# Performance work log

Measured on AMD Instinct MI355X. Metric: run time of the kernel, lower is better.

Reference implementation:

```python
import jax, jax.numpy as jnp
import numpy as np

NEG_SLOPE = 0.2  # PyG GATConv default negative_slope


def _add_self_loops(edge_index, num_nodes):
    # PyG GATConv add_self_loops=True default
    loop = jnp.arange(num_nodes, dtype=edge_index.dtype)
    src = jnp.concatenate([edge_index[0], loop])
    dst = jnp.concatenate([edge_index[1], loop])
    return src, dst


def _gat_layer(x, src, dst, W, att_src, att_dst, bias, heads, out_ch):
    """One PyG-style GATConv layer (concat=True).
    x: [N, F_in]; W: [F_in, heads*out_ch]; att_*: [heads, out_ch]; bias: [heads*out_ch].
    """
    N = x.shape[0]
    h = (x @ W).reshape(N, heads, out_ch)               # [N, H, C]
    a_src = jnp.einsum('nhc,hc->nh', h, att_src)        # [N, H]
    a_dst = jnp.einsum('nhc,hc->nh', h, att_dst)        # [N, H]
    logits = jax.nn.leaky_relu(a_src[src] + a_dst[dst], NEG_SLOPE)  # [E, H]
    # segment softmax over destination neighborhoods
    m = jax.ops.segment_max(logits, dst, num_segments=N)            # [N, H]
    e = jnp.exp(logits - m[dst])                                     # [E, H]
    s = jax.ops.segment_sum(e, dst, num_segments=N)                  # [N, H]
    alpha = e / s[dst]                                               # [E, H]
    # scatter-aggregate weighted source features
    out = jax.ops.segment_sum(alpha[:, :, None] * h[src], dst, num_segments=N)  # [N, H, C]
    return out.reshape(N, heads * out_ch) + bias


def setup_inputs() -> dict:
    key = jax.random.key(0)
    ks = jax.random.split(key, 10)
    N, E = 50000, 800000
    F_in, HID, H, NC = 128, 64, 4, 10
    x = jax.random.normal(ks[0], (N, F_in), dtype=jnp.float32)
    edge_index = jax.random.randint(ks[1], (2, E), 0, N, dtype=jnp.int64)
    sc1 = 1.0 / np.sqrt(F_in)
    sc2 = 1.0 / np.sqrt(HID * H)
    return {
        'x': x,
        'edge_index': edge_index,
        'W1': jax.random.normal(ks[2], (F_in, H * HID), dtype=jnp.float32) * sc1,
        'att_src1': jax.random.normal(ks[3], (H, HID), dtype=jnp.float32) * sc1,
        'att_dst1': jax.random.normal(ks[4], (H, HID), dtype=jnp.float32) * sc1,
        'b1': jnp.zeros((H * HID,), dtype=jnp.float32),
        'W2': jax.random.normal(ks[5], (H * HID, NC), dtype=jnp.float32) * sc2,
        'att_src2': jax.random.normal(ks[6], (1, NC), dtype=jnp.float32) * sc2,
        'att_dst2': jax.random.normal(ks[7], (1, NC), dtype=jnp.float32) * sc2,
        'b2': jnp.zeros((NC,), dtype=jnp.float32),
    }


def reference(x, edge_index, W1, att_src1, att_dst1, b1, W2, att_src2, att_dst2, b2):
    N = x.shape[0]
    src, dst = _add_self_loops(edge_index, N)
    h = _gat_layer(x, src, dst, W1, att_src1, att_dst1, b1, heads=4, out_ch=64)
    h = jax.nn.elu(h)
    out = _gat_layer(h, src, dst, W2, att_src2, att_dst2, b2, heads=1, out_ch=10)
    return out
```

## Files before the change

### kernel.cpp

```cpp
#include <hip/hip_runtime.h>
#include <hip/hip_fp16.h>
#include <math.h>

#define NEG_SLOPE 0.2f
#define LOG2E 1.44269504088896f

#if __has_builtin(__builtin_amdgcn_exp2f)
#define EXP2(x) __builtin_amdgcn_exp2f(x)
#else
#define EXP2(x) exp2f(x)
#endif

typedef _Float16 half8 __attribute__((ext_vector_type(8)));
typedef float floatx4 __attribute__((ext_vector_type(4)));

__global__ __launch_bounds__(256) void prep1(const float* __restrict__ W1,
                                             half8* __restrict__ Bpack,
                                             int* __restrict__ deg, int N) {
  if (blockIdx.x < 16) {
    int tid = blockIdx.x * 256 + threadIdx.x;
    int l = tid & 63;
    int ksnt = tid >> 6;
    int ks = ksnt & 3;
    int nt = ksnt >> 2;
    int col = nt * 16 + (l & 15);
    int krow = ks * 32 + (l >> 4) * 8;
    half8 v;
#pragma unroll
    for (int j = 0; j < 8; j++) v[j] = (_Float16)W1[(krow + j) * 256 + col];
    Bpack[tid] = v;
  } else {
    int i = (blockIdx.x - 16) * 256 + threadIdx.x;
    if (i < N) deg[i] = 0;
  }
}

__global__ __launch_bounds__(256) void phase2(
    const float* __restrict__ x, const half8* __restrict__ Bpack,
    const float* __restrict__ att_s, const float* __restrict__ att_d,
    __half* __restrict__ h1, float* __restrict__ a1s, float* __restrict__ a1d,
    const int* __restrict__ dst, int* __restrict__ deg,
    int N, int E, int gemmBlocks, int histBlocks) {
  if ((int)blockIdx.x >= gemmBlocks) {
    int b = blockIdx.x - gemmBlocks;
    for (int e = b * 256 + threadIdx.x; e < E; e += histBlocks * 256)
      atomicAdd(deg + dst[e], 1);
    return;
  }
  const int wave = threadIdx.x >> 6, lane = threadIdx.x & 63;
  const int quad = lane >> 4, li = lane & 15;
  const int n0 = (blockIdx.x * 4 + wave) * 16;
  if (n0 >= N) return;
  floatx4 acc[16];
#pragma unroll
  for (int t = 0; t < 16; t++) acc[t] = (floatx4){0.f, 0.f, 0.f, 0.f};
  const float* xrow = x + (size_t)(n0 + li) * 128;
#pragma unroll
  for (int ks = 0; ks < 4; ks++) {
    float4 xa = *(const float4*)(xrow + ks * 32 + quad * 8);
    float4 xb = *(const float4*)(xrow + ks * 32 + quad * 8 + 4);
    half8 a;
    a[0] = (_Float16)xa.x; a[1] = (_Float16)xa.y;
    a[2] = (_Float16)xa.z; a[3] = (_Float16)xa.w;
    a[4] = (_Float16)xb.x; a[5] = (_Float16)xb.y;
    a[6] = (_Float16)xb.z; a[7] = (_Float16)xb.w;
#pragma unroll
    for (int nt = 0; nt < 16; nt++) {
      half8 b = Bpack[(nt * 4 + ks) * 64 + lane];
      acc[nt] = __builtin_amdgcn_mfma_f32_16x16x32_f16(a, b, acc[nt], 0, 0, 0);
    }
  }
#pragma unroll
  for (int nt = 0; nt < 16; nt++) {
#pragma unroll
    for (int r = 0; r < 4; r++) {
      h1[(size_t)(n0 + quad * 4 + r) * 256 + nt * 16 + li] = __float2half(acc[nt][r]);
    }
  }
  float as_f[16], ad_f[16];
#pragma unroll
  for (int nt = 0; nt < 16; nt++) {
    as_f[nt] = att_s[nt * 16 + li];
    ad_f[nt] = att_d[nt * 16 + li];
  }
#pragma unroll
  for (int r = 0; r < 4; r++) {
    int node = n0 + quad * 4 + r;
#pragma unroll
    for (int h = 0; h < 4; h++) {
      float vs = 0.f, vd = 0.f;
#pragma unroll
      for (int ntl = 0; ntl < 4; ntl++) {
        int nt = h * 4 + ntl;
        vs = fmaf(acc[nt][r], as_f[nt], vs);
        vd = fmaf(acc[nt][r], ad_f[nt], vd);
      }
#pragma unroll
      for (int off = 8; off > 0; off >>= 1) {
        vs += __shfl_down(vs, off, 16);
        vd += __shfl_down(vd, off, 16);
      }
      if (li == 0) {
        a1s[node * 4 + h] = vs * LOG2E;
        a1d[node * 4 + h] = vd * LOG2E;
      }
    }
  }
}

__global__ void scan_local(const int* __restrict__ deg, int* __restrict__ excl,
                           int* __restrict__ bsum, int N) {
  __shared__ int s[256];
  int i = blockIdx.x * 256 + threadIdx.x;
  int v = (i < N) ? deg[i] + 1 : 0;
  s[threadIdx.x] = v;
  __syncthreads();
  for (int off = 1; off < 256; off <<= 1) {
    int t = (threadIdx.x >= off) ? s[threadIdx.x - off] : 0;
    __syncthreads();
    s[threadIdx.x] += t;
    __syncthreads();
  }
  if (i < N) excl[i] = s[threadIdx.x] - v;
  if (threadIdx.x == 255) bsum[blockIdx.x] = s[255];
}

__global__ void scan_bsum(int* __restrict__ bsum, int nb) {
  __shared__ int s[256];
  int v = (threadIdx.x < nb) ? bsum[threadIdx.x] : 0;
  s[threadIdx.x] = v;
  __syncthreads();
  for (int off = 1; off < 256; off <<= 1) {
    int t = (threadIdx.x >= off) ? s[threadIdx.x - off] : 0;
    __syncthreads();
    s[threadIdx.x] += t;
    __syncthreads();
  }
  if (threadIdx.x < nb) bsum[threadIdx.x] = s[threadIdx.x] - v;
}

__global__ void scan_add(const int* __restrict__ excl, const int* __restrict__ bsum,
                         int* __restrict__ rowptr, int* __restrict__ cursor,
                         int* __restrict__ elist, int N, int ET) {
  int i = blockIdx.x * 256 + threadIdx.x;
  if (i < N) {
    int r = excl[i] + bsum[blockIdx.x];
    rowptr[i] = r;
    elist[r] = i;
    cursor[i] = r + 1;
  }
  if (i == 0) rowptr[N] = ET;
}

__global__ void scatter_edges(const int* __restrict__ src, const int* __restrict__ dst,
                              int* __restrict__ cursor, int* __restrict__ elist, int E) {
  int e = blockIdx.x * 256 + threadIdx.x;
  if (e >= E) return;
  int pos = atomicAdd(cursor + dst[e], 1);
  elist[pos] = src[e];
}

__global__ __launch_bounds__(256) void agg1_fused(
    const int* __restrict__ rowptr, const int* __restrict__ elist,
    const __half* __restrict__ h1, const float* __restrict__ a1s,
    const float* __restrict__ a1d, const float* __restrict__ b1,
    const float* __restrict__ W2, const float* __restrict__ as2,
    const float* __restrict__ ad2, __half* __restrict__ h2,
    float* __restrict__ a2s, float* __restrict__ a2d, int N) {
  __shared__ float w2s[64 * 41];
  const int t = threadIdx.x;
  for (int i = t; i < 2560; i += 256) {
    int ch = i / 10, jj = i - ch * 10;
    w2s[(ch >> 2) * 41 + (ch & 3) * 10 + jj] = W2[i];
  }
  __syncthreads();

  const int wave = t >> 6, lane = t & 63;
  const int n = blockIdx.x * 4 + wave;
  if (n >= N) return;
  const int row = rowptr[n];
  const int deg = rowptr[n + 1] - row;
  const int* el = elist + row;
  const int hidx = lane >> 4;
  const float adh = a1d[n * 4 + hidx];

  float den = 0.f;
  float acc0 = 0.f, acc1 = 0.f, acc2 = 0.f, acc3 = 0.f;
  int j = 0;
  for (; j + 8 <= deg; j += 8) {
    int ss[8];
#pragma unroll
    for (int u = 0; u < 8; u++) ss[u] = el[j + u];
    float lv[8];
    uint2 uv[8];
#pragma unroll
    for (int u = 0; u < 8; u++) {
      lv[u] = a1s[ss[u] * 4 + hidx];
      uv[u] = *(const uint2*)(h1 + (size_t)ss[u] * 256 + lane * 4);
    }
#pragma unroll
    for (int u = 0; u < 8; u++) {
      float l = lv[u] + adh;
      float e = EXP2(fmaxf(l, NEG_SLOPE * l));
      den += e;
      float2 a = __half22float2(*(const __half2*)&uv[u].x);
      float2 b = __half22float2(*(const __half2*)&uv[u].y);
      acc0 = fmaf(e, a.x, acc0); acc1 = fmaf(e, a.y, acc1);
      acc2 = fmaf(e, b.x, acc2); acc3 = fmaf(e, b.y, acc3);
    }
  }
  for (; j + 4 <= deg; j += 4) {
    int ss[4];
#pragma unroll
    for (int u = 0; u < 4; u++) ss[u] = el[j + u];
    float lv[4];
    uint2 uv[4];
#pragma unroll
    for (int u = 0; u < 4; u++) {
      lv[u] = a1s[ss[u] * 4 + hidx];
      uv[u] = *(const uint2*)(h1 + (size_t)ss[u] * 256 + lane * 4);
    }
#pragma unroll
    for (int u = 0; u < 4; u++) {
      float l = lv[u] + adh;
      float e = EXP2(fmaxf(l, NEG_SLOPE * l));
      den += e;
      float2 a = __half22float2(*(const __half2*)&uv[u].x);
      float2 b = __half22float2(*(const __half2*)&uv[u].y);
      acc0 = fmaf(e, a.x, acc0); acc1 = fmaf(e, a.y, acc1);
      acc2 = fmaf(e, b.x, acc2); acc3 = fmaf(e, b.y, acc3);
    }
  }
  for (; j < deg; j++) {
    int s0 = el[j];
    float l0 = a1s[s0 * 4 + hidx] + adh;
    uint2 u0 = *(const uint2*)(h1 + (size_t)s0 * 256 + lane * 4);
    float e0 = EXP2(fmaxf(l0, NEG_SLOPE * l0));
    den += e0;
    float2 a = __half22float2(*(const __half2*)&u0.x);
    float2 b = __half22float2(*(const __half2*)&u0.y);
    acc0 = fmaf(e0, a.x, acc0); acc1 = fmaf(e0, a.y, acc1);
    acc2 = fmaf(e0, b.x, acc2); acc3 = fmaf(e0, b.y, acc3);
  }

  float inv = 1.0f / den;
  float4 bb = *(const float4*)(b1 + lane * 4);
  float c0 = fmaf(acc0, inv, bb.x);
  float c1 = fmaf(acc1, inv, bb.y);
  float c2 = fmaf(acc2, inv, bb.z);
  float c3 = fmaf(acc3, inv, bb.w);
  c0 = c0 > 0.f ? c0 : expm1f(c0);
  c1 = c1 > 0.f ? c1 : expm1f(c1);
  c2 = c2 > 0.f ? c2 : expm1f(c2);
  c3 = c3 > 0.f ? c3 : expm1f(c3);
  const float* w0 = w2s + lane * 41;
  float p[10];
#pragma unroll
  for (int jj = 0; jj < 10; jj++)
    p[jj] = fmaf(c0, w0[jj], fmaf(c1, w0[10 + jj], fmaf(c2, w0[20 + jj], c3 * w0[30 + jj])));
#pragma unroll
  for (int jj = 0; jj < 10; jj++) {
#pragma unroll
    for (int off = 32; off > 0; off >>= 1) p[jj] += __shfl_down(p[jj], off, 64);
  }
  if (lane == 0) {
    float ds = 0.f, dd = 0.f;
#pragma unroll
    for (int jj = 0; jj < 10; jj++) {
      h2[(size_t)n * 16 + jj] = __float2half(p[jj]);
      ds = fmaf(p[jj], as2[jj], ds);
      dd = fmaf(p[jj], ad2[jj], dd);
    }
    a2s[n] = ds * LOG2E;
    a2d[n] = dd * LOG2E;
  }
}

__global__ __launch_bounds__(256) void agg2_csr(
    const int* __restrict__ rowptr, const int* __restrict__ elist,
    const __half* __restrict__ h2, const float* __restrict__ a2s,
    const float* __restrict__ a2d, const float* __restrict__ b2,
    float* __restrict__ out, int N) {
  int wave = threadIdx.x >> 6, lane = threadIdx.x & 63;
  int n = blockIdx.x * 4 + wave;
  if (n >= N) return;
  int row = rowptr[n];
  int deg = rowptr[n + 1] - row;
  const int* el = elist + row;
  float ad = a2d[n];
  int g = lane / 10;
  int c = lane - g * 10;
  float den = 0.f, acc = 0.f;
  if (g < 6) {
    int jj = g;
    for (; jj + 6 < deg; jj += 12) {
      int sA = el[jj], sB = el[jj + 6];
      float lA = a2s[sA] + ad;
      float lB = a2s[sB] + ad;
      __half hA = h2[(size_t)sA * 16 + c];
      __half hB = h2[(size_t)sB * 16 + c];
      float eA = EXP2(fmaxf(lA, NEG_SLOPE * lA));
      float eB = EXP2(fmaxf(lB, NEG_SLOPE * lB));
      den += eA + eB;
      acc = fmaf(eA, __half2float(hA), fmaf(eB, __half2float(hB), acc));
    }
    for (; jj < deg; jj += 6) {
      int s = el[jj];
      float l = a2s[s] + ad;
      float ev = EXP2(fmaxf(l, NEG_SLOPE * l));
      den += ev;
      acc = fmaf(ev, __half2float(h2[(size_t)s * 16 + c]), acc);
    }
  }
  acc += __shfl_down(acc, 30, 64);
  den += __shfl_down(den, 30, 64);
  acc += __shfl_down(acc, 10, 64) + __shfl_down(acc, 20, 64);
  den += __shfl_down(den, 10, 64) + __shfl_down(den, 20, 64);
  if (lane < 10) out[(size_t)n * 10 + lane] = acc / den + b2[lane];
}

extern "C" void kernel_launch(void* const* d_in, const int* in_sizes, int n_in,
                              void* d_out, int out_size, void* d_ws, size_t ws_size,
                              hipStream_t stream) {
  const float* x = (const float*)d_in[0];
  const int* ei = (const int*)d_in[1];
  const float* W1 = (const float*)d_in[2];
  const float* as1 = (const float*)d_in[3];
  const float* ad1 = (const float*)d_in[4];
  const float* b1 = (const float*)d_in[5];
  const float* W2 = (const float*)d_in[6];
  const float* as2 = (const float*)d_in[7];
  const float* ad2 = (const float*)d_in[8];
  const float* b2 = (const float*)d_in[9];
  float* out = (float*)d_out;

  const int N = in_sizes[0] / 128;
  const int E = in_sizes[1] / 2;
  const int ET = E + N;
  const int* srcp = ei;
  const int* dstp = ei + E;

  char* ws = (char*)d_ws;
  size_t off = 0;
  auto alloc = [&](size_t nbytes) {
    char* p = ws + off;
    off += (nbytes + 255) & ~(size_t)255;
    return p;
  };
  __half* h1 = (__half*)alloc((size_t)N * 256 * 2);
  half8* Bpack = (half8*)alloc((size_t)4096 * 16);
  float* a1s = (float*)alloc((size_t)N * 4 * 4);
  float* a1d = (float*)alloc((size_t)N * 4 * 4);
  __half* h2 = (__half*)alloc((size_t)N * 16 * 2);
  float* a2sv = (float*)alloc((size_t)N * 4);
  float* a2dv = (float*)alloc((size_t)N * 4);
  int* deg = (int*)alloc((size_t)N * 4);
  int* excl = (int*)alloc((size_t)N * 4);
  int* bsum = (int*)alloc(256 * 4);
  int* rowptr = (int*)alloc((size_t)(N + 1) * 4);
  int* cursor = (int*)alloc((size_t)N * 4);
  int* elist = (int*)alloc((size_t)ET * 4);

  const int nb = (N + 255) / 256;
  const int gemmBlocks = (N / 16 + 3) / 4;
  const int histBlocks = 512;

  prep1<<<16 + nb, 256, 0, stream>>>(W1, Bpack, deg, N);
  phase2<<<gemmBlocks + histBlocks, 256, 0, stream>>>(
      x, Bpack, as1, ad1, h1, a1s, a1d, dstp, deg, N, E, gemmBlocks, histBlocks);
  scan_local<<<nb, 256, 0, stream>>>(deg, excl, bsum, N);
  scan_bsum<<<1, 256, 0, stream>>>(bsum, nb);
  scan_add<<<nb, 256, 0, stream>>>(excl, bsum, rowptr, cursor, elist, N, ET);
  scatter_edges<<<(E + 255) / 256, 256, 0, stream>>>(srcp, dstp, cursor, elist, E);
  agg1_fused<<<(N + 3) / 4, 256, 0, stream>>>(rowptr, elist, h1, a1s, a1d, b1, W2,
                                              as2, ad2, h2, a2sv, a2dv, N);
  agg2_csr<<<(N + 3) / 4, 256, 0, stream>>>(rowptr, elist, h2, a2sv, a2dv, b2, out, N);
}
```

Before: 295.9 us.

## Record atomic ranks in histogram, pad CSR rows, merge scan kernels

The degree histogram now stores each edge's atomicAdd return value as its rank. The scatter then writes edges directly to rowptr+1+rank, with no second atomic pass through a cursor array. Row lengths are padded to multiples of four so aggregation can read neighbor indices with aligned int4 loads. The block-sum scan is folded into the add kernel, which removes one launch. The cost is an extra E-sized rank array plus a larger elist, and the degree is read from the deg array rather than from rowptr differences.

```diff
diff --git a/kernel.cpp b/kernel.cpp
--- a/kernel.cpp
+++ b/kernel.cpp
@@ -39,12 +39,12 @@
     const float* __restrict__ x, const half8* __restrict__ Bpack,
     const float* __restrict__ att_s, const float* __restrict__ att_d,
     __half* __restrict__ h1, float* __restrict__ a1s, float* __restrict__ a1d,
-    const int* __restrict__ dst, int* __restrict__ deg,
+    const int* __restrict__ dst, int* __restrict__ deg, int* __restrict__ rank,
     int N, int E, int gemmBlocks, int histBlocks) {
   if ((int)blockIdx.x >= gemmBlocks) {
     int b = blockIdx.x - gemmBlocks;
     for (int e = b * 256 + threadIdx.x; e < E; e += histBlocks * 256)
-      atomicAdd(deg + dst[e], 1);
+      rank[e] = atomicAdd(deg + dst[e], 1);
     return;
   }
   const int wave = threadIdx.x >> 6, lane = threadIdx.x & 63;
@@ -112,7 +112,7 @@
                            int* __restrict__ bsum, int N) {
   __shared__ int s[256];
   int i = blockIdx.x * 256 + threadIdx.x;
-  int v = (i < N) ? deg[i] + 1 : 0;
+  int v = (i < N) ? ((deg[i] + 1 + 3) & ~3) : 0;
   s[threadIdx.x] = v;
   __syncthreads();
   for (int off = 1; off < 256; off <<= 1) {
@@ -125,7 +125,9 @@
   if (threadIdx.x == 255) bsum[blockIdx.x] = s[255];
 }
 
-__global__ void scan_bsum(int* __restrict__ bsum, int nb) {
+__global__ void scan_add2(const int* __restrict__ excl, const int* __restrict__ bsum,
+                          int* __restrict__ rowptr, int* __restrict__ elist,
+                          int N, int nb) {
   __shared__ int s[256];
   int v = (threadIdx.x < nb) ? bsum[threadIdx.x] : 0;
   s[threadIdx.x] = v;
@@ -136,37 +138,32 @@
     s[threadIdx.x] += t;
     __syncthreads();
   }
-  if (threadIdx.x < nb) bsum[threadIdx.x] = s[threadIdx.x] - v;
-}
-
-__global__ void scan_add(const int* __restrict__ excl, const int* __restrict__ bsum,
-                         int* __restrict__ rowptr, int* __restrict__ cursor,
-                         int* __restrict__ elist, int N, int ET) {
+  __syncthreads();
+  int base = (blockIdx.x > 0) ? s[blockIdx.x - 1] : 0;
   int i = blockIdx.x * 256 + threadIdx.x;
   if (i < N) {
-    int r = excl[i] + bsum[blockIdx.x];
+    int r = excl[i] + base;
     rowptr[i] = r;
     elist[r] = i;
-    cursor[i] = r + 1;
-  }
-  if (i == 0) rowptr[N] = ET;
-}
-
-__global__ void scatter_edges(const int* __restrict__ src, const int* __restrict__ dst,
-                              int* __restrict__ cursor, int* __restrict__ elist, int E) {
+  }
+}
+
+__global__ void scatter2(const int* __restrict__ src, const int* __restrict__ dst,
+                         const int* __restrict__ rank, const int* __restrict__ rowptr,
+                         int* __restrict__ elist, int E) {
   int e = blockIdx.x * 256 + threadIdx.x;
   if (e >= E) return;
-  int pos = atomicAdd(cursor + dst[e], 1);
-  elist[pos] = src[e];
+  elist[rowptr[dst[e]] + 1 + rank[e]] = src[e];
 }
 
 __global__ __launch_bounds__(256) void agg1_fused(
-    const int* __restrict__ rowptr, const int* __restrict__ elist,
-    const __half* __restrict__ h1, const float* __restrict__ a1s,
-    const float* __restrict__ a1d, const float* __restrict__ b1,
-    const float* __restrict__ W2, const float* __restrict__ as2,
-    const float* __restrict__ ad2, __half* __restrict__ h2,
-    float* __restrict__ a2s, float* __restrict__ a2d, int N) {
+    const int* __restrict__ rowptr, const int* __restrict__ degp,
+    const int* __restrict__ elist, const __half* __restrict__ h1,
+    const float* __restrict__ a1s, const float* __restrict__ a1d,
+    const float* __restrict__ b1, const float* __restrict__ W2,
+    const float* __restrict__ as2, const float* __restrict__ ad2,
+    __half* __restrict__ h2, float* __restrict__ a2s, float* __restrict__ a2d,
+    int N) {
   __shared__ float w2s[64 * 41];
   const int t = threadIdx.x;
   for (int i = t; i < 2560; i += 256) {
@@ -179,7 +176,7 @@
   const int n = blockIdx.x * 4 + wave;
   if (n >= N) return;
   const int row = rowptr[n];
-  const int deg = rowptr[n + 1] - row;
+  const int deg = degp[n] + 1;
   const int* el = elist + row;
   const int hidx = lane >> 4;
   const float adh = a1d[n * 4 + hidx];
@@ -188,9 +185,9 @@
   float acc0 = 0.f, acc1 = 0.f, acc2 = 0.f, acc3 = 0.f;
   int j = 0;
   for (; j + 8 <= deg; j += 8) {
-    int ss[8];
-#pragma unroll
-    for (int u = 0; u < 8; u++) ss[u] = el[j + u];
+    int4 eA = *(const int4*)(el + j);
+    int4 eB = *(const int4*)(el + j + 4);
+    int ss[8] = {eA.x, eA.y, eA.z, eA.w, eB.x, eB.y, eB.z, eB.w};
     float lv[8];
     uint2 uv[8];
 #pragma unroll
@@ -210,9 +207,8 @@
     }
   }
   for (; j + 4 <= deg; j += 4) {
-    int ss[4];
-#pragma unroll
-    for (int u = 0; u < 4; u++) ss[u] = el[j + u];
+    int4 eA = *(const int4*)(el + j);
+    int ss[4] = {eA.x, eA.y, eA.z, eA.w};
     float lv[4];
     uint2 uv[4];
 #pragma unroll
@@ -277,15 +273,15 @@
 }
 
 __global__ __launch_bounds__(256) void agg2_csr(
-    const int* __restrict__ rowptr, const int* __restrict__ elist,
-    const __half* __restrict__ h2, const float* __restrict__ a2s,
-    const float* __restrict__ a2d, const float* __restrict__ b2,
-    float* __restrict__ out, int N) {
+    const int* __restrict__ rowptr, const int* __restrict__ degp,
+    const int* __restrict__ elist, const __half* __restrict__ h2,
+    const float* __restrict__ a2s, const float* __restrict__ a2d,
+    const float* __restrict__ b2, float* __restrict__ out, int N) {
   int wave = threadIdx.x >> 6, lane = threadIdx.x & 63;
   int n = blockIdx.x * 4 + wave;
   if (n >= N) return;
   int row = rowptr[n];
-  int deg = rowptr[n + 1] - row;
+  int deg = degp[n] + 1;
   const int* el = elist + row;
   float ad = a2d[n];
   int g = lane / 10;
@@ -336,7 +332,6 @@
 
   const int N = in_sizes[0] / 128;
   const int E = in_sizes[1] / 2;
-  const int ET = E + N;
   const int* srcp = ei;
   const int* dstp = ei + E;
 
@@ -358,8 +353,8 @@
   int* excl = (int*)alloc((size_t)N * 4);
   int* bsum = (int*)alloc(256 * 4);
   int* rowptr = (int*)alloc((size_t)(N + 1) * 4);
-  int* cursor = (int*)alloc((size_t)N * 4);
-  int* elist = (int*)alloc((size_t)ET * 4);
+  int* rank = (int*)alloc((size_t)E * 4);
+  int* elist = (int*)alloc((size_t)(E + 4 * (size_t)N) * 4);
 
   const int nb = (N + 255) / 256;
   const int gemmBlocks = (N / 16 + 3) / 4;
@@ -367,12 +362,12 @@
 
   prep1<<<16 + nb, 256, 0, stream>>>(W1, Bpack, deg, N);
   phase2<<<gemmBlocks + histBlocks, 256, 0, stream>>>(
-      x, Bpack, as1, ad1, h1, a1s, a1d, dstp, deg, N, E, gemmBlocks, histBlocks);
+      x, Bpack, as1, ad1, h1, a1s, a1d, dstp, deg, rank, N, E, gemmBlocks, histBlocks);
   scan_local<<<nb, 256, 0, stream>>>(deg, excl, bsum, N);
-  scan_bsum<<<1, 256, 0, stream>>>(bsum, nb);
-  scan_add<<<nb, 256, 0, stream>>>(excl, bsum, rowptr, cursor, elist, N, ET);
-  scatter_edges<<<(E + 255) / 256, 256, 0, stream>>>(srcp, dstp, cursor, elist, E);
-  agg1_fused<<<(N + 3) / 4, 256, 0, stream>>>(rowptr, elist, h1, a1s, a1d, b1, W2,
-                                              as2, ad2, h2, a2sv, a2dv, N);
-  agg2_csr<<<(N + 3) / 4, 256, 0, stream>>>(rowptr, elist, h2, a2sv, a2dv, b2, out, N);
-}
+  scan_add2<<<nb, 256, 0, stream>>>(excl, bsum, rowptr, elist, N, nb);
+  scatter2<<<(E + 255) / 256, 256, 0, stream>>>(srcp, dstp, rank, rowptr, elist, E);
+  agg1_fused<<<(N + 3) / 4, 256, 0, stream>>>(rowptr, deg, elist, h1, a1s, a1d, b1,
+                                              W2, as2, ad2, h2, a2sv, a2dv, N);
+  agg2_csr<<<(N + 3) / 4, 256, 0, stream>>>(rowptr, deg, elist, h2, a2sv, a2dv, b2,
+                                            out, N);
+}
```

New measurement: 267.5 us. 1.11x faster.
